# Optimization experiments

Measured on AMD Instinct MI355X. Metric: run time of the kernel, lower is better.

Reference implementation:

```python
import jax, jax.numpy as jnp
import numpy as np

# Static problem sizes (see shape_source)
B, SX, SY = 256, 256, 70          # graphs, encoder nodes/graph, decoder nodes/graph
F, EMB, H = 512, 256, 256          # f_size, emb_size, h_size
VOCAB = 256
E = 4 * B * SY                     # 71680 edges
N_SLT = 4                          # SltEdgeTypes
N_SRT = 8                          # len(SrtEdgeTypes)


def setup_inputs() -> dict:
    key = jax.random.key(0)
    ks = jax.random.split(key, 24)
    s = 0.02
    inp = {
        'x': jax.random.normal(ks[0], (B * SX, F), jnp.float32),
        'x_batch': jnp.repeat(jnp.arange(B, dtype=jnp.int64), SX),
        'tgt_y': jax.random.randint(ks[1], (B * SY,), 0, VOCAB, jnp.int64),
        'tgt_edge_index': jax.random.randint(ks[2], (2, E), 0, B * SY, jnp.int64),
        'tgt_edge_type': jax.random.randint(ks[3], (E,), 0, N_SLT, jnp.int64),
        'tgt_y_batch': jnp.repeat(jnp.arange(B, dtype=jnp.int64), SY),
        'embeds': jax.random.normal(ks[4], (VOCAB, EMB), jnp.float32) * s,
    }
    dims = [(EMB, H), (H, H), (H, EMB)]
    k = 5
    for l, (din, dout) in enumerate(dims, start=1):
        inp[f'W_in{l}'] = jax.random.normal(ks[k + 0], (din, dout), jnp.float32) * s
        inp[f'Wq{l}'] = jax.random.normal(ks[k + 1], (dout, F), jnp.float32) * s
        inp[f'Wv{l}'] = jax.random.normal(ks[k + 2], (F, dout), jnp.float32) * s
        inp[f'Ee{l}'] = jax.random.normal(ks[k + 3], (N_SLT, dout), jnp.float32) * s
        k += 4
    inp['lin_z_w'] = jax.random.normal(ks[k], (EMB, VOCAB), jnp.float32) * s
    inp['lin_z_b'] = jnp.zeros((VOCAB,), jnp.float32)
    inp['lin_g_w'] = jax.random.normal(ks[k + 1], (2 * EMB, N_SRT), jnp.float32) * s
    inp['lin_g_b'] = jnp.zeros((N_SRT,), jnp.float32)
    return inp


def gcn_dec_layer(x_b, y, src, tgt, etype, W_in, Wq, Wv, Ee):
    """Edge-type-conditioned message passing + cross-attention onto encoder x.
    x_b: [B,SX,F]; y: [Ny,din]. Returns ([Ny,dout], alpha [B,SY,SX])."""
    h = y @ W_in                                   # [Ny, dout]
    m = h[src] + Ee[etype]                         # gather + type embedding
    agg = jax.ops.segment_sum(m, tgt, num_segments=y.shape[0])
    q = (h @ Wq).reshape(B, SY, F)                 # query into encoder space
    logits = jnp.einsum('bqf,bkf->bqk', q, x_b) / jnp.sqrt(jnp.float32(F))
    alpha = jax.nn.softmax(logits, axis=-1)        # [B,SY,SX]
    ctx = jnp.einsum('bqk,bkf->bqf', alpha, x_b) @ Wv  # [B,SY,dout]
    out = jax.nn.relu(h + agg + ctx.reshape(h.shape[0], -1))
    return out, alpha


def reference(x, x_batch, tgt_y, tgt_edge_index, tgt_edge_type, tgt_y_batch,
              embeds, W_in1, Wq1, Wv1, Ee1, W_in2, Wq2, Wv2, Ee2,
              W_in3, Wq3, Wv3, Ee3, lin_z_w, lin_z_b, lin_g_w, lin_g_b):
    x_b = x.reshape(B, SX, F)
    src, tgt = tgt_edge_index[0], tgt_edge_index[1]
    y = embeds[tgt_y]                              # [Ny, EMB]
    y, a1 = gcn_dec_layer(x_b, y, src, tgt, tgt_edge_type, W_in1, Wq1, Wv1, Ee1)
    y, a2 = gcn_dec_layer(x_b, y, src, tgt, tgt_edge_type, W_in2, Wq2, Wv2, Ee2)
    y, a3 = gcn_dec_layer(x_b, y, src, tgt, tgt_edge_type, W_in3, Wq3, Wv3, Ee3)
    y_score = y @ lin_z_w + lin_z_b                # [Ny, VOCAB]
    ef = y[tgt_edge_index]                         # [2, E, EMB]
    ef = jnp.transpose(ef, (1, 0, 2)).reshape(E, 2 * EMB)
    y_edge_rel_score = ef @ lin_g_w + lin_g_b      # [E, N_SRT]
    return (y, y_score, y_edge_rel_score, a1, a2, a3)
```

## Files before the change

kernel.cpp:

```cpp
#include <hip/hip_runtime.h>
#include <cstddef>
#include <cstdint>

#define B_    256
#define SX_   256
#define SY_   70
#define F_    512
#define EMB_  256
#define NY_   (B_*SY_)
#define NE_   (4*B_*SY_)

typedef short s16x8 __attribute__((ext_vector_type(8)));
typedef float f32x4 __attribute__((ext_vector_type(4)));
typedef unsigned short us4 __attribute__((ext_vector_type(4)));
typedef unsigned short us8 __attribute__((ext_vector_type(8)));

__device__ __forceinline__ unsigned short f2bf(float f) {
    unsigned u = __builtin_bit_cast(unsigned, f);
    u += 0x7fffu + ((u >> 16) & 1u);
    return (unsigned short)(u >> 16);
}
__device__ __forceinline__ float bf2f(unsigned short b) {
    unsigned u = ((unsigned)b) << 16;
    return __builtin_bit_cast(float, u);
}

template<int EPI, int SWZ>
__global__ __launch_bounds__(256, 2)
void gemm_mfma(const unsigned short* __restrict__ A, int lda, long sAb,
               const unsigned short* __restrict__ Bt, int ldb, long sBb,
               float* __restrict__ Cf, int ldc, long sCfb,
               unsigned short* __restrict__ Cb, int ldcb, long sCbb,
               const float* __restrict__ aux1, long sAux,
               int M, int K, float scale, int nx, int ny)
{
    __shared__ unsigned short As[128 * 64];
    __shared__ unsigned short Bs[128 * 64];
    char* AsB = (char*)As;
    char* BsB = (char*)Bs;
    const int tid = threadIdx.x;
    int bxi, byi, z;
    if (SWZ) {
        const int nwg = gridDim.x;
        const int bid = blockIdx.x;
        const int wg = (bid & 7) * (nwg >> 3) + (bid >> 3);
        bxi = wg % nx;
        byi = (wg / nx) % ny;
        z   = wg / (nx * ny);
    } else {
        bxi = blockIdx.x; byi = blockIdx.y; z = blockIdx.z;
    }
    A  += (size_t)z * sAb;
    Bt += (size_t)z * sBb;
    const char* auxp = (const char*)aux1 + (size_t)z * sAux;
    const int bm = byi * 128, bn = bxi * 128;
    const int lane = tid & 63;
    const int w = tid >> 6, wr = w >> 1, wc = w & 1;
    const int l15 = lane & 15, lq = lane >> 4;

    f32x4 acc[4][4];
    const f32x4 z4 = {0.f, 0.f, 0.f, 0.f};
#pragma unroll
    for (int m = 0; m < 4; ++m)
#pragma unroll
        for (int n = 0; n < 4; ++n) acc[m][n] = z4;

    for (int k0 = 0; k0 < K; k0 += 64) {
#pragma unroll
        for (int i = 0; i < 4; ++i) {
            const int row = i * 32 + (tid >> 3);
            const int k8  = (tid & 7) ^ (row & 7);
            int ra = bm + row; ra = (ra < M) ? ra : (M - 1);
            const unsigned short* g = A + (size_t)ra * lda + k0 + k8 * 8;
            __builtin_amdgcn_global_load_lds(
                (const __attribute__((address_space(1))) unsigned int*)g,
                (__attribute__((address_space(3))) unsigned int*)(AsB + i * 4096 + tid * 16),
                16, 0, 0);
        }
#pragma unroll
        for (int i = 0; i < 4; ++i) {
            const int row = i * 32 + (tid >> 3);
            const int k8  = (tid & 7) ^ (row & 7);
            const unsigned short* g = Bt + (size_t)(bn + row) * ldb + k0 + k8 * 8;
            __builtin_amdgcn_global_load_lds(
                (const __attribute__((address_space(1))) unsigned int*)g,
                (__attribute__((address_space(3))) unsigned int*)(BsB + i * 4096 + tid * 16),
                16, 0, 0);
        }
        __syncthreads();
#pragma unroll
        for (int kk = 0; kk < 2; ++kk) {
            s16x8 af[4], bf[4];
#pragma unroll
            for (int m = 0; m < 4; ++m) {
                const int row = wr * 64 + m * 16 + l15;
                const int slot = (kk * 4 + lq) ^ (row & 7);
                af[m] = *(const s16x8*)(AsB + row * 128 + slot * 16);
            }
#pragma unroll
            for (int n = 0; n < 4; ++n) {
                const int col = wc * 64 + n * 16 + l15;
                const int slot = (kk * 4 + lq) ^ (col & 7);
                bf[n] = *(const s16x8*)(BsB + col * 128 + slot * 16);
            }
#pragma unroll
            for (int m = 0; m < 4; ++m)
#pragma unroll
                for (int n = 0; n < 4; ++n)
                    acc[m][n] = __builtin_amdgcn_mfma_f32_16x16x32_bf16(
                        af[m], bf[n], acc[m][n], 0, 0, 0);
        }
        __syncthreads();
    }

    float* cf = Cf ? Cf + (size_t)z * sCfb : nullptr;
    unsigned short* cb = Cb ? Cb + (size_t)z * sCbb : nullptr;
#pragma unroll
    for (int m = 0; m < 4; ++m) {
#pragma unroll
        for (int n = 0; n < 4; ++n) {
            const int col = bn + wc * 64 + n * 16 + l15;
            f32x4 v = acc[m][n];
#pragma unroll
            for (int r = 0; r < 4; ++r) {
                const int gr = bm + wr * 64 + m * 16 + lq * 4 + r;
                if (gr >= M) continue;
                float o = v[r] * scale;
                if (EPI == 4) o += ((const float*)auxp)[col];
                if (EPI == 6) {
                    o += bf2f(((const unsigned short*)auxp)[(size_t)gr * ldc + col]);
                    o = fmaxf(o, 0.f);
                }
                if (EPI == 7) {
                    if (col < 256) cb[(size_t)gr * ldcb + col] = f2bf(o);
                    else ((unsigned short*)cf)[(size_t)gr * 512 + (col - 256)] = f2bf(o);
                } else {
                    if (cf) cf[(size_t)gr * ldc + col] = o;
                    if (cb) cb[(size_t)gr * ldcb + col] = f2bf(o);
                }
            }
        }
    }
}

__global__ __launch_bounds__(512, 1)
void attn_logits_sm(const unsigned short* __restrict__ Q,
                    const unsigned short* __restrict__ X,
                    float* __restrict__ Aout,
                    unsigned short* __restrict__ Ab,
                    float scale)
{
    __shared__ unsigned short As[128 * 64];
    __shared__ unsigned short Bs[256 * 64];
    __shared__ float red[4][2][64];
    char* AsB = (char*)As;
    char* BsB = (char*)Bs;
    const int tid = threadIdx.x;
    const int z = blockIdx.x;
    const unsigned short* Qb = Q + (size_t)z * SY_ * F_;
    const unsigned short* Xb = X + (size_t)z * SX_ * F_;
    const int lane = tid & 63;
    const int w = tid >> 6, wr = w >> 2, wc = w & 3;
    const int l15 = lane & 15, lq = lane >> 4;

    f32x4 acc[4][4];
    const f32x4 z4 = {0.f, 0.f, 0.f, 0.f};
#pragma unroll
    for (int m = 0; m < 4; ++m)
#pragma unroll
        for (int n = 0; n < 4; ++n) acc[m][n] = z4;

    for (int k0 = 0; k0 < F_; k0 += 64) {
#pragma unroll
        for (int i = 0; i < 2; ++i) {
            const int row = i * 64 + (tid >> 3);
            const int k8  = (tid & 7) ^ (row & 7);
            const int ra = (row < SY_) ? row : (SY_ - 1);
            const unsigned short* g = Qb + (size_t)ra * F_ + k0 + k8 * 8;
            __builtin_amdgcn_global_load_lds(
                (const __attribute__((address_space(1))) unsigned int*)g,
                (__attribute__((address_space(3))) unsigned int*)(AsB + i * 8192 + tid * 16),
                16, 0, 0);
        }
#pragma unroll
        for (int i = 0; i < 4; ++i) {
            const int row = i * 64 + (tid >> 3);
            const int k8  = (tid & 7) ^ (row & 7);
            const unsigned short* g = Xb + (size_t)row * F_ + k0 + k8 * 8;
            __builtin_amdgcn_global_load_lds(
                (const __attribute__((address_space(1))) unsigned int*)g,
                (__attribute__((address_space(3))) unsigned int*)(BsB + i * 8192 + tid * 16),
                16, 0, 0);
        }
        __syncthreads();
#pragma unroll
        for (int kk = 0; kk < 2; ++kk) {
            s16x8 af[4], bf[4];
#pragma unroll
            for (int m = 0; m < 4; ++m) {
                const int row = wr * 64 + m * 16 + l15;
                const int slot = (kk * 4 + lq) ^ (row & 7);
                af[m] = *(const s16x8*)(AsB + row * 128 + slot * 16);
            }
#pragma unroll
            for (int n = 0; n < 4; ++n) {
                const int col = wc * 64 + n * 16 + l15;
                const int slot = (kk * 4 + lq) ^ (col & 7);
                bf[n] = *(const s16x8*)(BsB + col * 128 + slot * 16);
            }
#pragma unroll
            for (int m = 0; m < 4; ++m)
#pragma unroll
                for (int n = 0; n < 4; ++n)
                    acc[m][n] = __builtin_amdgcn_mfma_f32_16x16x32_bf16(
                        af[m], bf[n], acc[m][n], 0, 0, 0);
        }
        __syncthreads();
    }

#pragma unroll
    for (int m = 0; m < 4; ++m)
#pragma unroll
        for (int n = 0; n < 4; ++n)
#pragma unroll
            for (int r = 0; r < 4; ++r) acc[m][n][r] *= scale;

    float rmax[4][4];
#pragma unroll
    for (int m = 0; m < 4; ++m)
#pragma unroll
        for (int r = 0; r < 4; ++r) {
            float mx = acc[m][0][r];
#pragma unroll
            for (int n = 1; n < 4; ++n) mx = fmaxf(mx, acc[m][n][r]);
            mx = fmaxf(mx, __shfl_xor(mx, 1));
            mx = fmaxf(mx, __shfl_xor(mx, 2));
            mx = fmaxf(mx, __shfl_xor(mx, 4));
            mx = fmaxf(mx, __shfl_xor(mx, 8));
            rmax[m][r] = mx;
        }
    if (l15 == 0) {
#pragma unroll
        for (int m = 0; m < 4; ++m)
#pragma unroll
            for (int r = 0; r < 4; ++r)
                red[wc][wr][m * 16 + lq * 4 + r] = rmax[m][r];
    }
    __syncthreads();
    float rtot[4][4];
#pragma unroll
    for (int m = 0; m < 4; ++m)
#pragma unroll
        for (int r = 0; r < 4; ++r) {
            const int lr = m * 16 + lq * 4 + r;
            rtot[m][r] = fmaxf(fmaxf(red[0][wr][lr], red[1][wr][lr]),
                               fmaxf(red[2][wr][lr], red[3][wr][lr]));
        }
    __syncthreads();
    float rsum[4][4];
#pragma unroll
    for (int m = 0; m < 4; ++m)
#pragma unroll
        for (int r = 0; r < 4; ++r) {
            float s = 0.f;
#pragma unroll
            for (int n = 0; n < 4; ++n) {
                float e = __expf(acc[m][n][r] - rtot[m][r]);
                acc[m][n][r] = e;
                s += e;
            }
            s += __shfl_xor(s, 1);
            s += __shfl_xor(s, 2);
            s += __shfl_xor(s, 4);
            s += __shfl_xor(s, 8);
            rsum[m][r] = s;
        }
    if (l15 == 0) {
#pragma unroll
        for (int m = 0; m < 4; ++m)
#pragma unroll
            for (int r = 0; r < 4; ++r)
                red[wc][wr][m * 16 + lq * 4 + r] = rsum[m][r];
    }
    __syncthreads();
    float* ao = Aout + (size_t)z * SY_ * SX_;
    unsigned short* ab = Ab + (size_t)z * SY_ * SX_;
#pragma unroll
    for (int m = 0; m < 4; ++m)
#pragma unroll
        for (int r = 0; r < 4; ++r) {
            const int lr = m * 16 + lq * 4 + r;
            const int row = wr * 64 + lr;
            if (row >= SY_) continue;
            const float inv = 1.0f / (red[0][wr][lr] + red[1][wr][lr] +
                                      red[2][wr][lr] + red[3][wr][lr]);
#pragma unroll
            for (int n = 0; n < 4; ++n) {
                const int col = wc * 64 + n * 16 + l15;
                const float o = acc[m][n][r] * inv;
                ao[(size_t)row * SX_ + col] = o;
                ab[(size_t)row * SX_ + col] = f2bf(o);
            }
        }
}

__global__ __launch_bounds__(256)
void conv_x(const float* __restrict__ in, unsigned short* __restrict__ out, int n8)
{
    for (int i = blockIdx.x * 256 + threadIdx.x; i < n8; i += 2048 * 256) {
        float4 a = ((const float4*)in)[i * 2];
        float4 b = ((const float4*)in)[i * 2 + 1];
        us8 o = { f2bf(a.x), f2bf(a.y), f2bf(a.z), f2bf(a.w),
                  f2bf(b.x), f2bf(b.y), f2bf(b.z), f2bf(b.w) };
        ((us8*)out)[i] = o;
    }
}

struct WAll {
    const float* src[10];
    unsigned short* dst[10];
    int R[10];
    int C[10];
};

__global__ __launch_bounds__(256)
void conv_wT_all(WAll d)
{
    const int z = blockIdx.z;
    const int R = d.R[z], C = d.C[z];
    const int c0 = blockIdx.x * 64, r0 = blockIdx.y * 64;
    if (c0 >= C || r0 >= R) return;
    const float* in = d.src[z];
    unsigned short* outT = d.dst[z];
    __shared__ unsigned short t[64][65];
    const int r = threadIdx.x >> 4, cq = (threadIdx.x & 15) << 2;
#pragma unroll
    for (int i = 0; i < 4; ++i) {
        const int rr = r + i * 16;
        float4 v = *(const float4*)(in + (size_t)(r0 + rr) * C + c0 + cq);
        t[rr][cq + 0] = f2bf(v.x); t[rr][cq + 1] = f2bf(v.y);
        t[rr][cq + 2] = f2bf(v.z); t[rr][cq + 3] = f2bf(v.w);
    }
    __syncthreads();
    const int c = threadIdx.x >> 2, sq = (threadIdx.x & 3) << 4;
    us8 o0, o1;
#pragma unroll
    for (int i = 0; i < 8; ++i) { o0[i] = t[sq + i][c]; o1[i] = t[sq + 8 + i][c]; }
    *(us8*)(outT + (size_t)(c0 + c) * R + r0 + sq) = o0;
    *(us8*)(outT + (size_t)(c0 + c) * R + r0 + sq + 8) = o1;
}

__global__ __launch_bounds__(256)
void gather_embed(const float* __restrict__ embeds, const int* __restrict__ tgt_y,
                  unsigned short* __restrict__ yb)
{
    const int i = blockIdx.x * 8 + (threadIdx.x >> 5);
    const int c8 = (threadIdx.x & 31) * 8;
    const int v = tgt_y[i];
    const float* p = embeds + (size_t)v * 256 + c8;
    float4 a = *(const float4*)p;
    float4 b = *(const float4*)(p + 4);
    us8 o = { f2bf(a.x), f2bf(a.y), f2bf(a.z), f2bf(a.w),
              f2bf(b.x), f2bf(b.y), f2bf(b.z), f2bf(b.w) };
    *(us8*)(yb + (size_t)i * 256 + c8) = o;
}

__global__ __launch_bounds__(256)
void edge_deg(const int* __restrict__ tgt, int* __restrict__ deg)
{
    const int e = blockIdx.x * 256 + threadIdx.x;
    if (e < NE_) atomicAdd(&deg[tgt[e]], 1);
}

__global__ __launch_bounds__(1024)
void scan_off(const int* __restrict__ deg, int* __restrict__ off, int* __restrict__ cursor)
{
    __shared__ int ls[1024];
    const int t = threadIdx.x;
    const int base = t * 18;
    int local[18];
    int s = 0;
#pragma unroll
    for (int i = 0; i < 18; ++i) {
        const int idx = base + i;
        const int v = (idx < NY_) ? deg[idx] : 0;
        local[i] = s; s += v;
    }
    ls[t] = s;
    __syncthreads();
    for (int d = 1; d < 1024; d <<= 1) {
        int v = (t >= d) ? ls[t - d] : 0;
        __syncthreads();
        ls[t] += v;
        __syncthreads();
    }
    const int excl = (t == 0) ? 0 : ls[t - 1];
#pragma unroll
    for (int i = 0; i < 18; ++i) {
        const int idx = base + i;
        if (idx < NY_) {
            const int o = excl + local[i];
            off[idx] = o; cursor[idx] = o;
        }
    }
    if (t == 1023) off[NY_] = ls[1023];
}

__global__ __launch_bounds__(256)
void edge_fill(const int* __restrict__ tgt, int* __restrict__ cursor,
               int* __restrict__ elist)
{
    const int e = blockIdx.x * 256 + threadIdx.x;
    if (e >= NE_) return;
    const int pos = atomicAdd(&cursor[tgt[e]], 1);
    elist[pos] = e;
}

__global__ __launch_bounds__(256)
void node_agg(const unsigned short* __restrict__ hb,
              const float* __restrict__ Ee,
              const int* __restrict__ src, const int* __restrict__ etype,
              const int* __restrict__ off, const int* __restrict__ elist,
              unsigned short* __restrict__ aggb)
{
    const int nid  = blockIdx.x * 4 + (threadIdx.x >> 6);
    const int lane = threadIdx.x & 63;
    const int c = lane * 4;
    const int k0 = off[nid], k1 = off[nid + 1];
    us4 sv = *(const us4*)(hb + (size_t)nid * 256 + c);
    float4 acc;
    acc.x = bf2f(sv[0]); acc.y = bf2f(sv[1]);
    acc.z = bf2f(sv[2]); acc.w = bf2f(sv[3]);
    int cnt0 = 0, cnt1 = 0, cnt2 = 0, cnt3 = 0;
    for (int k = k0; k < k1; ++k) {
        const int e = elist[k];
        const int sfrom = src[e];
        const int ty = etype[e];
        us4 hv = *(const us4*)(hb + (size_t)sfrom * 256 + c);
        acc.x += bf2f(hv[0]); acc.y += bf2f(hv[1]);
        acc.z += bf2f(hv[2]); acc.w += bf2f(hv[3]);
        cnt0 += (ty == 0); cnt1 += (ty == 1); cnt2 += (ty == 2); cnt3 += (ty == 3);
    }
    float4 e0 = *(const float4*)(Ee + c);
    float4 e1 = *(const float4*)(Ee + 256 + c);
    float4 e2 = *(const float4*)(Ee + 512 + c);
    float4 e3 = *(const float4*)(Ee + 768 + c);
    acc.x += cnt0 * e0.x + cnt1 * e1.x + cnt2 * e2.x + cnt3 * e3.x;
    acc.y += cnt0 * e0.y + cnt1 * e1.y + cnt2 * e2.y + cnt3 * e3.y;
    acc.z += cnt0 * e0.z + cnt1 * e1.z + cnt2 * e2.z + cnt3 * e3.z;
    acc.w += cnt0 * e0.w + cnt1 * e1.w + cnt2 * e2.w + cnt3 * e3.w;
    us4 o = { f2bf(acc.x), f2bf(acc.y), f2bf(acc.z), f2bf(acc.w) };
    *(us4*)(aggb + (size_t)nid * 256 + c) = o;
}

__global__ __launch_bounds__(256)
void edge_w(const float* __restrict__ y, const float* __restrict__ W,
            float* __restrict__ Y12)
{
    __shared__ float Ws[4096];
    __shared__ float ys[16][260];
    const int tid = threadIdx.x;
#pragma unroll
    for (int i = 0; i < 4; ++i)
        ((float4*)Ws)[i * 256 + tid] = ((const float4*)W)[i * 256 + tid];
    const int r = tid >> 4, seg = tid & 15;
    const int r0 = blockIdx.x * 16;
#pragma unroll
    for (int i = 0; i < 4; ++i) {
        const int c4 = seg + i * 16;
        *(float4*)&ys[r][c4 * 4] = *(const float4*)(y + (size_t)(r0 + r) * 256 + c4 * 4);
    }
    __syncthreads();
    const int j = tid & 15;
    const int row = tid >> 4;
    const float* Wcol = Ws + ((j < 8) ? j : (2048 + j - 8));
    float acc = 0.f;
#pragma unroll 4
    for (int c = 0; c < 256; ++c) acc = fmaf(ys[row][c], Wcol[c * 8], acc);
    Y12[(size_t)(r0 + row) * 16 + j] = acc;
}

__global__ __launch_bounds__(256)
void edge_gather(const float* __restrict__ Y12, const int* __restrict__ src,
                 const int* __restrict__ tgt, const float* __restrict__ bias,
                 float* __restrict__ esc)
{
    const int e = blockIdx.x * 256 + threadIdx.x;
    if (e >= NE_) return;
    const float* a = Y12 + (size_t)src[e] * 16;
    const float* b = Y12 + (size_t)tgt[e] * 16 + 8;
    float4 a0 = ((const float4*)a)[0], a1 = ((const float4*)a)[1];
    float4 b0 = ((const float4*)b)[0], b1 = ((const float4*)b)[1];
    float4 c0 = ((const float4*)bias)[0], c1 = ((const float4*)bias)[1];
    float4 o0, o1;
    o0.x = a0.x + b0.x + c0.x; o0.y = a0.y + b0.y + c0.y;
    o0.z = a0.z + b0.z + c0.z; o0.w = a0.w + b0.w + c0.w;
    o1.x = a1.x + b1.x + c1.x; o1.y = a1.y + b1.y + c1.y;
    o1.z = a1.z + b1.z + c1.z; o1.w = a1.w + b1.w + c1.w;
    ((float4*)(esc + (size_t)e * 8))[0] = o0;
    ((float4*)(esc + (size_t)e * 8))[1] = o1;
}

extern "C" void kernel_launch(void* const* d_in, const int* in_sizes, int n_in,
                              void* d_out, int out_size, void* d_ws, size_t ws_size,
                              hipStream_t stream)
{
    const float* x       = (const float*)d_in[0];
    const int*   tgt_y   = (const int*)d_in[2];
    const int*   eidx    = (const int*)d_in[3];
    const int*   etype   = (const int*)d_in[4];
    const float* embeds  = (const float*)d_in[6];
    const float* W_in[3] = {(const float*)d_in[7],  (const float*)d_in[11], (const float*)d_in[15]};
    const float* Wq[3]   = {(const float*)d_in[8],  (const float*)d_in[12], (const float*)d_in[16]};
    const float* Wv[3]   = {(const float*)d_in[9],  (const float*)d_in[13], (const float*)d_in[17]};
    const float* Ee[3]   = {(const float*)d_in[10], (const float*)d_in[14], (const float*)d_in[18]};
    const float* lin_z_w = (const float*)d_in[19];
    const float* lin_z_b = (const float*)d_in[20];
    const float* lin_g_w = (const float*)d_in[21];
    const float* lin_g_b = (const float*)d_in[22];
    const int* src = eidx;
    const int* tgt = eidx + NE_;

    float* out = (float*)d_out;
    float* y_final = out;
    float* score   = out + 4587520;
    float* esc     = out + 9175040;
    float* aout[3] = {out + 9748480, out + 14336000, out + 18923520};

    char* wsb = (char*)d_ws;
    unsigned short* xb     = (unsigned short*)(wsb + 0);
    unsigned short* xvTall = (unsigned short*)(wsb + 67108864);
    unsigned short* hb     = (unsigned short*)(wsb + 167772160);
    unsigned short* aggb   = (unsigned short*)(wsb + 176947200);
    unsigned short* qb     = (unsigned short*)(wsb + 186122240);
    unsigned short* yb     = (unsigned short*)(wsb + 204472320);
    char* wt = wsb + 213647360;
    unsigned short* wcatT[3], *wqT[3], *wvT[3];
    for (int l = 0; l < 3; ++l) {
        wcatT[l] = (unsigned short*)(wt + l * 393216);
        wqT[l]   = (unsigned short*)(wt + 1179648 + l * 262144);
        wvT[l]   = (unsigned short*)(wt + 1966080 + l * 262144);
    }
    unsigned short* lzT = (unsigned short*)(wt + 2752512);
    char* extra = wsb + 216530944;
    float* Y12    = (float*)extra;
    int*   deg    = (int*)(extra + 1146880);
    int*   off    = (int*)(extra + 1218560);
    int*   cursor = (int*)(extra + 1290244);
    int*   elist  = (int*)(extra + 1361924);

    hipMemsetAsync(deg, 0, NY_ * sizeof(int), stream);
    edge_deg<<<280, 256, 0, stream>>>(tgt, deg);
    scan_off<<<1, 1024, 0, stream>>>(deg, off, cursor);
    edge_fill<<<280, 256, 0, stream>>>(tgt, cursor, elist);

    conv_x<<<2048, 256, 0, stream>>>(x, xb, 4194304);
    WAll wd;
    for (int l = 0; l < 3; ++l) {
        wd.src[l]     = W_in[l]; wd.dst[l]     = wcatT[l]; wd.R[l]     = 256; wd.C[l]     = 256;
        wd.src[3 + l] = Wq[l];   wd.dst[3 + l] = wqT[l];   wd.R[3 + l] = 256; wd.C[3 + l] = 512;
        wd.src[6 + l] = Wv[l];   wd.dst[6 + l] = wvT[l];   wd.R[6 + l] = 512; wd.C[6 + l] = 256;
    }
    wd.src[9] = lin_z_w; wd.dst[9] = lzT; wd.R[9] = 256; wd.C[9] = 256;
    conv_wT_all<<<dim3(8, 8, 10), 256, 0, stream>>>(wd);
    gather_embed<<<2240, 256, 0, stream>>>(embeds, tgt_y, yb);

    gemm_mfma<0, 0><<<dim3(2, 4, 3), 256, 0, stream>>>(
        wqT[0], 256, 131072L,  wcatT[0], 256, 196608L,
        nullptr, 0, 0,  wcatT[0] + 65536, 256, 196608L,
        nullptr, 0, 512, 256, 1.f, 0, 0);

    gemm_mfma<0, 1><<<3072, 256, 0, stream>>>(
        wvT[0], 512, 0,  xb, 512, (long)SX_ * F_,
        nullptr, 0, 0,  xvTall, 256, 768L * 256,
        nullptr, 0, 768, 512, 1.f, 2, 6);

    const float qscale = 0.044194173824159216f;
    for (int l = 0; l < 3; ++l) {
        gemm_mfma<7, 0><<<dim3(6, 140, 1), 256, 0, stream>>>(
            yb, 256, 0,  wcatT[l], 256, 0,
            (float*)qb, 512, 0,  hb, 256, 0,
            nullptr, 0, NY_, 256, 1.f, 0, 0);
        node_agg<<<4480, 256, 0, stream>>>(hb, Ee[l], src, etype, off, elist, aggb);
        attn_logits_sm<<<256, 512, 0, stream>>>(qb, xb, aout[l], hb, qscale);
        gemm_mfma<6, 0><<<dim3(2, 1, B_), 256, 0, stream>>>(
            hb, 256, (long)SY_ * SX_,  xvTall + (size_t)l * 65536, 256, 768L * 256,
            (l == 2) ? y_final : nullptr, 256, (long)SY_ * EMB_,
            yb, 256, (long)SY_ * EMB_,
            (const float*)aggb, (long)SY_ * EMB_ * 2, SY_, 256, 1.f, 0, 0);
    }
    gemm_mfma<4, 0><<<dim3(2, 140, 1), 256, 0, stream>>>(
        yb, 256, 0,  lzT, 256, 0,
        score, 256, 0,  nullptr, 0, 0,
        lin_z_b, 0, NY_, 256, 1.f, 0, 0);
    edge_w<<<1120, 256, 0, stream>>>(y_final, lin_g_w, Y12);
    edge_gather<<<280, 256, 0, stream>>>(Y12, src, tgt, lin_g_b, esc);
}
```

Before: 467.5 us.

## Fuse attention softmax with PV GEMM and residual-relu epilogue

Merges the attention logits/softmax kernel with the following alpha x (X·Wv) GEMM, so the normalized bf16 alpha tile stays in a swizzled LDS buffer instead of being written to global memory and re-read. The fused kernel then adds the aggregated message and applies ReLU, writing y directly. This removes one kernel launch per layer and the alpha round trip through global memory. In exchange it needs 64KB of extra LDS per block, at one block per CU, and the PV GEMM now runs on only 256 blocks instead of 512.

Result: faster. 449.0 us (-4.0%).

```diff
diff --git a/kernel.cpp b/kernel.cpp
--- a/kernel.cpp
+++ b/kernel.cpp
@@ -127,10 +127,6 @@
                 if (gr >= M) continue;
                 float o = v[r] * scale;
                 if (EPI == 4) o += ((const float*)auxp)[col];
-                if (EPI == 6) {
-                    o += bf2f(((const unsigned short*)auxp)[(size_t)gr * ldc + col]);
-                    o = fmaxf(o, 0.f);
-                }
                 if (EPI == 7) {
                     if (col < 256) cb[(size_t)gr * ldcb + col] = f2bf(o);
                     else ((unsigned short*)cf)[(size_t)gr * 512 + (col - 256)] = f2bf(o);
@@ -144,21 +140,28 @@
 }
 
 __global__ __launch_bounds__(512, 1)
-void attn_logits_sm(const unsigned short* __restrict__ Q,
-                    const unsigned short* __restrict__ X,
-                    float* __restrict__ Aout,
-                    unsigned short* __restrict__ Ab,
-                    float scale)
+void attn_pv(const unsigned short* __restrict__ Q,
+             const unsigned short* __restrict__ X,
+             const unsigned short* __restrict__ XV,
+             long sXVb,
+             const unsigned short* __restrict__ aggb,
+             float* __restrict__ Aout,
+             unsigned short* __restrict__ Yb,
+             float* __restrict__ Yf,
+             float scale)
 {
     __shared__ unsigned short As[128 * 64];
     __shared__ unsigned short Bs[256 * 64];
+    __shared__ unsigned short Al[128 * 256];
     __shared__ float red[4][2][64];
     char* AsB = (char*)As;
     char* BsB = (char*)Bs;
+    char* AlB = (char*)Al;
     const int tid = threadIdx.x;
     const int z = blockIdx.x;
-    const unsigned short* Qb = Q + (size_t)z * SY_ * F_;
-    const unsigned short* Xb = X + (size_t)z * SX_ * F_;
+    const unsigned short* Qb  = Q + (size_t)z * SY_ * F_;
+    const unsigned short* Xb  = X + (size_t)z * SX_ * F_;
+    const unsigned short* xvb = XV + (size_t)z * sXVb;
     const int lane = tid & 63;
     const int w = tid >> 6, wr = w >> 2, wc = w & 3;
     const int l15 = lane & 15, lq = lane >> 4;
@@ -284,22 +287,84 @@
     }
     __syncthreads();
     float* ao = Aout + (size_t)z * SY_ * SX_;
-    unsigned short* ab = Ab + (size_t)z * SY_ * SX_;
 #pragma unroll
     for (int m = 0; m < 4; ++m)
 #pragma unroll
         for (int r = 0; r < 4; ++r) {
             const int lr = m * 16 + lq * 4 + r;
             const int row = wr * 64 + lr;
-            if (row >= SY_) continue;
             const float inv = 1.0f / (red[0][wr][lr] + red[1][wr][lr] +
                                       red[2][wr][lr] + red[3][wr][lr]);
 #pragma unroll
             for (int n = 0; n < 4; ++n) {
                 const int col = wc * 64 + n * 16 + l15;
                 const float o = acc[m][n][r] * inv;
-                ao[(size_t)row * SX_ + col] = o;
-                ab[(size_t)row * SX_ + col] = f2bf(o);
+                if (row < SY_) ao[(size_t)row * SX_ + col] = o;
+                *(unsigned short*)(AlB + row * 512 +
+                    (((col >> 3) ^ (row & 7)) << 4) + ((col & 7) << 1)) = f2bf(o);
+            }
+        }
+    __syncthreads();
+
+    f32x4 oac[4][4];
+#pragma unroll
+    for (int m = 0; m < 4; ++m)
+#pragma unroll
+        for (int n = 0; n < 4; ++n) oac[m][n] = z4;
+
+    for (int ks = 0; ks < 4; ++ks) {
+        const int k0 = ks * 64;
+#pragma unroll
+        for (int i = 0; i < 4; ++i) {
+            const int row = i * 64 + (tid >> 3);
+            const int k8  = (tid & 7) ^ (row & 7);
+            const unsigned short* g = xvb + (size_t)row * 256 + k0 + k8 * 8;
+            __builtin_amdgcn_global_load_lds(
+                (const __attribute__((address_space(1))) unsigned int*)g,
+                (__attribute__((address_space(3))) unsigned int*)(BsB + i * 8192 + tid * 16),
+                16, 0, 0);
+        }
+        __syncthreads();
+#pragma unroll
+        for (int kk = 0; kk < 2; ++kk) {
+            s16x8 af[4], bf[4];
+#pragma unroll
+            for (int m = 0; m < 4; ++m) {
+                const int row = wr * 64 + m * 16 + l15;
+                const int chunk = (k0 >> 3) + kk * 4 + lq;
+                af[m] = *(const s16x8*)(AlB + row * 512 + ((chunk ^ (row & 7)) << 4));
+            }
+#pragma unroll
+            for (int n = 0; n < 4; ++n) {
+                const int col = wc * 64 + n * 16 + l15;
+                const int slot = (kk * 4 + lq) ^ (col & 7);
+                bf[n] = *(const s16x8*)(BsB + col * 128 + slot * 16);
+            }
+#pragma unroll
+            for (int m = 0; m < 4; ++m)
+#pragma unroll
+                for (int n = 0; n < 4; ++n)
+                    oac[m][n] = __builtin_amdgcn_mfma_f32_16x16x32_bf16(
+                        af[m], bf[n], oac[m][n], 0, 0, 0);
+        }
+        __syncthreads();
+    }
+
+#pragma unroll
+    for (int m = 0; m < 4; ++m)
+#pragma unroll
+        for (int n = 0; n < 4; ++n) {
+            const int col = wc * 64 + n * 16 + l15;
+            f32x4 v = oac[m][n];
+#pragma unroll
+            for (int r = 0; r < 4; ++r) {
+                const int row = wr * 64 + m * 16 + lq * 4 + r;
+                if (row >= SY_) continue;
+                const size_t node = (size_t)z * SY_ + row;
+                float o = v[r] + bf2f(aggb[node * 256 + col]);
+                o = fmaxf(o, 0.f);
+                Yb[node * 256 + col] = f2bf(o);
+                if (Yf) Yf[node * 256 + col] = o;
             }
         }
 }
@@ -582,12 +647,9 @@
             (float*)qb, 512, 0,  hb, 256, 0,
             nullptr, 0, NY_, 256, 1.f, 0, 0);
         node_agg<<<4480, 256, 0, stream>>>(hb, Ee[l], src, etype, off, elist, aggb);
-        attn_logits_sm<<<256, 512, 0, stream>>>(qb, xb, aout[l], hb, qscale);
-        gemm_mfma<6, 0><<<dim3(2, 1, B_), 256, 0, stream>>>(
-            hb, 256, (long)SY_ * SX_,  xvTall + (size_t)l * 65536, 256, 768L * 256,
-            (l == 2) ? y_final : nullptr, 256, (long)SY_ * EMB_,
-            yb, 256, (long)SY_ * EMB_,
-            (const float*)aggb, (long)SY_ * EMB_ * 2, SY_, 256, 1.f, 0, 0);
+        attn_pv<<<256, 512, 0, stream>>>(
+            qb, xb, xvTall + (size_t)l * 65536, 768L * 256,
+            aggb, aout[l], yb, (l == 2) ? y_final : nullptr, qscale);
     }
     gemm_mfma<4, 0><<<dim3(2, 140, 1), 256, 0, stream>>>(
         yb, 256, 0,  lzT, 256, 0,
```
